# Optimization experiments

Measured on AMD Instinct MI355X. Metric: run time of the kernel, lower is better.

The kernel has to match this reference:

```python
import jax, jax.numpy as jnp
import numpy as np

N, E, D = 50000, 500000, 128


def layer_norm(x, w, b, eps=1e-5):
    mu = jnp.mean(x, axis=-1, keepdims=True)
    var = jnp.var(x, axis=-1, keepdims=True)
    return (x - mu) * jax.lax.rsqrt(var + eps) * w + b


def setup_inputs() -> dict:
    key = jax.random.key(0)
    ks = jax.random.split(key, 8)
    z = jax.random.normal(ks[0], (N, D), dtype=jnp.float32)
    pot_arcs = jax.random.randint(ks[1], (E, 2), 0, N, dtype=jnp.int64)
    s = 1.0 / np.sqrt(D)
    lin1_w = jax.random.uniform(ks[2], (D, D), jnp.float32, -s, s)
    lin1_b = jax.random.uniform(ks[3], (D,), jnp.float32, -s, s)
    lin2_w = jax.random.uniform(ks[4], (D, D), jnp.float32, -s, s)
    lin2_b = jax.random.uniform(ks[5], (D,), jnp.float32, -s, s)
    bil_w = jax.random.uniform(ks[6], (1, D, D), jnp.float32, -s, s)
    bil_b = jax.random.uniform(ks[7], (1,), jnp.float32, -s, s)
    norm_w = jnp.ones((D,), jnp.float32)
    norm_b = jnp.zeros((D,), jnp.float32)
    return {"z": z, "pot_arcs": pot_arcs, "lin1_w": lin1_w, "lin1_b": lin1_b,
            "lin2_w": lin2_w, "lin2_b": lin2_b, "bil_w": bil_w, "bil_b": bil_b,
            "norm_w": norm_w, "norm_b": norm_b}


def reference(z, pot_arcs, lin1_w, lin1_b, lin2_w, lin2_b, bil_w, bil_b, norm_w, norm_b):
    # shared LayerNorm on all nodes
    zn = layer_norm(z, norm_w, norm_b)                     # [N, D]
    x1 = zn[pot_arcs[:, 0]]                                # [E, D] gather heads
    x2 = zn[pot_arcs[:, 1]]                                # [E, D] gather tails
    # lin -> relu -> layernorm (dropout = identity at eval)
    h1 = layer_norm(jax.nn.relu(x1 @ lin1_w.T + lin1_b), norm_w, norm_b)
    h2 = layer_norm(jax.nn.relu(x2 @ lin2_w.T + lin2_b), norm_w, norm_b)
    # bilinear score: out_e = h1_e^T W h2_e + b, W = bil_w[0]
    score = jnp.einsum('ed,df,ef->e', h1, bil_w[0], h2) + bil_b[0]
    return score                                           # [E]
```

## Files before the change

### kernel.cpp

```cpp
#include <hip/hip_runtime.h>

#define D 128
#define TM 64

typedef __attribute__((ext_vector_type(8))) short short8v;
typedef __attribute__((ext_vector_type(4))) float float4v;

__device__ __forceinline__ unsigned short f2bf(float f) {
    unsigned int u = __float_as_uint(f);
    u += 0x7FFFu + ((u >> 16) & 1u);
    return (unsigned short)(u >> 16);
}
__device__ __forceinline__ float bflo(int u) {
    return __uint_as_float(((unsigned int)u) << 16);
}
__device__ __forceinline__ float bfhi(int u) {
    return __uint_as_float(((unsigned int)u) & 0xFFFF0000u);
}

__global__ __launch_bounds__(256) void wconv(
    const float* __restrict__ w1, const float* __restrict__ w2,
    const float* __restrict__ wb, unsigned short* __restrict__ dst)
{
    int tid = blockIdx.x * 256 + threadIdx.x;
    int w = tid >> 11;
    int r = tid & 2047;
    int l = r & 63;
    int tk = r >> 6;
    int t = tk >> 2, ks = tk & 3;
    int n = t * 16 + (l & 15);
    int k = ks * 32 + (l >> 4) * 8;
    const float* src = (w == 0) ? w1 : (w == 1) ? w2 : wb;
    const float* p = src + n * D + k;
    float4 a = *(const float4*)p;
    float4 b = *(const float4*)(p + 4);
    union { int4 i4; unsigned short u[8]; } pk;
    pk.u[0] = f2bf(a.x); pk.u[1] = f2bf(a.y); pk.u[2] = f2bf(a.z); pk.u[3] = f2bf(a.w);
    pk.u[4] = f2bf(b.x); pk.u[5] = f2bf(b.y); pk.u[6] = f2bf(b.z); pk.u[7] = f2bf(b.w);
    *(int4*)(dst + (size_t)tid * 8) = pk.i4;
}

__global__ __launch_bounds__(256) void node_kernel(
    const float* __restrict__ z,
    const unsigned short* __restrict__ wfrag,
    const float* __restrict__ lin1_b, const float* __restrict__ lin2_b,
    const float* __restrict__ norm_w, const float* __restrict__ norm_b,
    unsigned short* __restrict__ T1, unsigned short* __restrict__ T2,
    int N)
{
    __shared__ unsigned short sa[TM][136];
    __shared__ unsigned short sh[TM][136];

    const int tid   = threadIdx.x;
    const int lane  = tid & 63;
    const int wave  = tid >> 6;
    const int n0    = blockIdx.x * TM;
    const int cg    = lane & 15;
    const int q     = lane >> 4;
    const int rbase = wave * 16;

    {
        const int c = cg * 8;
        float4 nw0 = *(const float4*)(norm_w + c);
        float4 nw1 = *(const float4*)(norm_w + c + 4);
        float4 nb0 = *(const float4*)(norm_b + c);
        float4 nb1 = *(const float4*)(norm_b + c + 4);
        #pragma unroll
        for (int it = 0; it < 4; ++it) {
            int rr = rbase + it * 4 + q;
            int n  = n0 + rr;
            int nc = (n < N) ? n : (N - 1);
            const float* zp = z + (size_t)nc * D + c;
            float4 v0 = *(const float4*)zp;
            float4 v1 = *(const float4*)(zp + 4);
            float s  = v0.x + v0.y + v0.z + v0.w + v1.x + v1.y + v1.z + v1.w;
            float qq = v0.x*v0.x + v0.y*v0.y + v0.z*v0.z + v0.w*v0.w
                     + v1.x*v1.x + v1.y*v1.y + v1.z*v1.z + v1.w*v1.w;
            #pragma unroll
            for (int m = 1; m <= 8; m <<= 1) {
                s  += __shfl_xor(s, m, 64);
                qq += __shfl_xor(qq, m, 64);
            }
            float mu  = s * (1.0f / D);
            float var = qq * (1.0f / D) - mu * mu;
            float rs  = rsqrtf(var + 1e-5f);
            union { int4 i4; unsigned short u[8]; } pk;
            pk.u[0] = f2bf((v0.x - mu) * rs * nw0.x + nb0.x);
            pk.u[1] = f2bf((v0.y - mu) * rs * nw0.y + nb0.y);
            pk.u[2] = f2bf((v0.z - mu) * rs * nw0.z + nb0.z);
            pk.u[3] = f2bf((v0.w - mu) * rs * nw0.w + nb0.w);
            pk.u[4] = f2bf((v1.x - mu) * rs * nw1.x + nb1.x);
            pk.u[5] = f2bf((v1.y - mu) * rs * nw1.y + nb1.y);
            pk.u[6] = f2bf((v1.z - mu) * rs * nw1.z + nb1.z);
            pk.u[7] = f2bf((v1.w - mu) * rs * nw1.w + nb1.w);
            *(int4*)&sa[rr][c] = pk.i4;
        }
    }

    float4v acc1[8], acc2[8];
    #pragma unroll
    for (int t = 0; t < 8; ++t) { acc1[t] = (float4v)(0.0f); acc2[t] = (float4v)(0.0f); }
    #pragma unroll
    for (int ks = 0; ks < 4; ++ks) {
        short8v a = *(const short8v*)&sa[rbase + cg][ks * 32 + q * 8];
        const short8v* wp = (const short8v*)wfrag + ks * 64 + lane;
        #pragma unroll
        for (int t = 0; t < 8; ++t) {
            acc1[t] = __builtin_amdgcn_mfma_f32_16x16x32_bf16(a, wp[t * 256],        acc1[t], 0, 0, 0);
            acc2[t] = __builtin_amdgcn_mfma_f32_16x16x32_bf16(a, wp[t * 256 + 2048], acc2[t], 0, 0, 0);
        }
    }

    auto epilogue = [&](float4v* acc, const float* lb, unsigned short (*dst)[136]) {
        float s[4] = {0, 0, 0, 0}, qs[4] = {0, 0, 0, 0};
        #pragma unroll
        for (int t = 0; t < 8; ++t) {
            float b = lb[t * 16 + cg];
            #pragma unroll
            for (int i = 0; i < 4; ++i) {
                float v = fmaxf(acc[t][i] + b, 0.0f);
                acc[t][i] = v;
                s[i] += v; qs[i] += v * v;
            }
        }
        #pragma unroll
        for (int i = 0; i < 4; ++i) {
            #pragma unroll
            for (int m = 1; m <= 8; m <<= 1) {
                s[i]  += __shfl_xor(s[i], m, 64);
                qs[i] += __shfl_xor(qs[i], m, 64);
            }
            float mu  = s[i] * (1.0f / D);
            float var = qs[i] * (1.0f / D) - mu * mu;
            s[i] = mu; qs[i] = rsqrtf(var + 1e-5f);
        }
        #pragma unroll
        for (int t = 0; t < 8; ++t) {
            int col = t * 16 + cg;
            float nw = norm_w[col], nb = norm_b[col];
            #pragma unroll
            for (int i = 0; i < 4; ++i)
                dst[rbase + q * 4 + i][col] = f2bf((acc[t][i] - s[i]) * qs[i] * nw + nb);
        }
    };

    auto copyout = [&](const unsigned short (*S)[136], unsigned short* dst) {
        int r = tid >> 2;
        int n = n0 + r;
        if (n < N) {
            #pragma unroll
            for (int j = 0; j < 4; ++j) {
                int c = (tid & 3) * 8 + j * 32;
                *(int4*)(dst + (size_t)n * D + c) = *(const int4*)&S[r][c];
            }
        }
    };

    epilogue(acc1, lin1_b, sh);
    copyout(sh, T1);
    epilogue(acc2, lin2_b, sa);

    #pragma unroll
    for (int t = 0; t < 8; ++t) acc1[t] = (float4v)(0.0f);
    #pragma unroll
    for (int ks = 0; ks < 4; ++ks) {
        short8v a = *(const short8v*)&sa[rbase + cg][ks * 32 + q * 8];
        const short8v* wp = (const short8v*)wfrag + 4096 + ks * 64 + lane;
        #pragma unroll
        for (int t = 0; t < 8; ++t)
            acc1[t] = __builtin_amdgcn_mfma_f32_16x16x32_bf16(a, wp[t * 256], acc1[t], 0, 0, 0);
    }
    #pragma unroll
    for (int t = 0; t < 8; ++t)
        #pragma unroll
        for (int i = 0; i < 4; ++i)
            sh[rbase + q * 4 + i][t * 16 + cg] = f2bf(acc1[t][i]);
    copyout(sh, T2);
}

__global__ __launch_bounds__(256) void arc_kernel(
    const int* __restrict__ arcs,
    const unsigned short* __restrict__ T1,
    const unsigned short* __restrict__ T2,
    const float* __restrict__ bil_b,
    float* __restrict__ out, int E)
{
    const int tid  = threadIdx.x;
    const int lane = tid & 63;
    long long gw = ((long long)blockIdx.x * 256 + tid) >> 6;
    long long e0 = gw * 32;
    int aidx = lane >> 2;
    int s    = lane & 3;

    long long ii = e0 * 2 + lane;
    long long iimax = (long long)E * 2 - 1;
    int iv = arcs[ii <= iimax ? ii : iimax];
    int a0A = __shfl(iv, aidx * 2, 64);
    int a1A = __shfl(iv, aidx * 2 + 1, 64);
    int a0B = __shfl(iv, 32 + aidx * 2, 64);
    int a1B = __shfl(iv, 32 + aidx * 2 + 1, 64);
    long long eA = e0 + aidx;
    long long eB = e0 + 16 + aidx;

    const int4* PA = (const int4*)(T1 + (size_t)a0A * D);
    const int4* QA = (const int4*)(T2 + (size_t)a1A * D);
    const int4* PB = (const int4*)(T1 + (size_t)a0B * D);
    const int4* QB = (const int4*)(T2 + (size_t)a1B * D);
    int4 xa0 = PA[s], xa1 = PA[s + 4], xa2 = PA[s + 8], xa3 = PA[s + 12];
    int4 ya0 = QA[s], ya1 = QA[s + 4], ya2 = QA[s + 8], ya3 = QA[s + 12];
    int4 xb0 = PB[s], xb1 = PB[s + 4], xb2 = PB[s + 8], xb3 = PB[s + 12];
    int4 yb0 = QB[s], yb1 = QB[s + 4], yb2 = QB[s + 8], yb3 = QB[s + 12];

    #define DOT4(a, b) (bflo(a.x)*bflo(b.x) + bfhi(a.x)*bfhi(b.x) + \
                        bflo(a.y)*bflo(b.y) + bfhi(a.y)*bfhi(b.y) + \
                        bflo(a.z)*bflo(b.z) + bfhi(a.z)*bfhi(b.z) + \
                        bflo(a.w)*bflo(b.w) + bfhi(a.w)*bfhi(b.w))

    float accA = 0.0f, accB = 0.0f;
    accA += DOT4(xa0, ya0); accA += DOT4(xa1, ya1);
    accA += DOT4(xa2, ya2); accA += DOT4(xa3, ya3);
    accB += DOT4(xb0, yb0); accB += DOT4(xb1, yb1);
    accB += DOT4(xb2, yb2); accB += DOT4(xb3, yb3);
    #undef DOT4

    accA += __shfl_xor(accA, 1, 64);
    accA += __shfl_xor(accA, 2, 64);
    accB += __shfl_xor(accB, 1, 64);
    accB += __shfl_xor(accB, 2, 64);

    if (s == 0) {
        float bb = bil_b[0];
        if (eA < E) out[eA] = accA + bb;
        if (eB < E) out[eB] = accB + bb;
    }
}

extern "C" void kernel_launch(void* const* d_in, const int* in_sizes, int n_in,
                              void* d_out, int out_size, void* d_ws, size_t ws_size,
                              hipStream_t stream) {
    const float* z      = (const float*)d_in[0];
    const int*   arcs   = (const int*)d_in[1];
    const float* lin1_w = (const float*)d_in[2];
    const float* lin1_b = (const float*)d_in[3];
    const float* lin2_w = (const float*)d_in[4];
    const float* lin2_b = (const float*)d_in[5];
    const float* bil_w  = (const float*)d_in[6];
    const float* bil_b  = (const float*)d_in[7];
    const float* norm_w = (const float*)d_in[8];
    const float* norm_b = (const float*)d_in[9];
    float* out = (float*)d_out;

    const int N = in_sizes[0] / D;
    const int E = in_sizes[1] / 2;

    unsigned short* wfrag = (unsigned short*)d_ws;
    unsigned short* T1 = wfrag + 3 * 16384;
    unsigned short* T2 = T1 + (size_t)N * D;

    wconv<<<24, 256, 0, stream>>>(lin1_w, lin2_w, bil_w, wfrag);

    node_kernel<<<(N + TM - 1) / TM, 256, 0, stream>>>(
        z, wfrag, lin1_b, lin2_b, norm_w, norm_b, T1, T2, N);

    long long waves = ((long long)E + 31) / 32;
    int blocks = (int)((waves + 3) / 4);
    arc_kernel<<<blocks, 256, 0, stream>>>(arcs, T1, T2, bil_b, out, E);
}
```

Baseline: 143.8 us.

## Double node-kernel row tile so each wave reuses weight fragments across two row tiles

Raises the node kernel's row tile from 64 to 128, so each wave computes two 16-row MFMA tiles. Each weight fragment loaded from global is then reused for both tiles, roughly halving weight traffic per node. The separate shared staging buffer is removed and the single buffer is reused for the epilogue and copy-out, which keeps LDS use flat. The costs are doubled accumulator register pressure and half as many blocks, which may leave the GPU less occupied for N=50000.

```diff
diff --git a/kernel.cpp b/kernel.cpp
--- a/kernel.cpp
+++ b/kernel.cpp
@@ -1,7 +1,7 @@
 #include <hip/hip_runtime.h>
 
 #define D 128
-#define TM 64
+#define TM 128
 
 typedef __attribute__((ext_vector_type(8))) short short8v;
 typedef __attribute__((ext_vector_type(4))) float float4v;
@@ -49,7 +49,6 @@
     int N)
 {
     __shared__ unsigned short sa[TM][136];
-    __shared__ unsigned short sh[TM][136];
 
     const int tid   = threadIdx.x;
     const int lane  = tid & 63;
@@ -57,7 +56,7 @@
     const int n0    = blockIdx.x * TM;
     const int cg    = lane & 15;
     const int q     = lane >> 4;
-    const int rbase = wave * 16;
+    const int rbase = wave * 32;
 
     {
         const int c = cg * 8;
@@ -66,7 +65,7 @@
         float4 nb0 = *(const float4*)(norm_b + c);
         float4 nb1 = *(const float4*)(norm_b + c + 4);
         #pragma unroll
-        for (int it = 0; it < 4; ++it) {
+        for (int it = 0; it < 8; ++it) {
             int rr = rbase + it * 4 + q;
             int n  = n0 + rr;
             int nc = (n < N) ? n : (N - 1);
@@ -97,29 +96,36 @@
         }
     }
 
-    float4v acc1[8], acc2[8];
-    #pragma unroll
-    for (int t = 0; t < 8; ++t) { acc1[t] = (float4v)(0.0f); acc2[t] = (float4v)(0.0f); }
+    float4v acc1[2][8], acc2[2][8];
+    #pragma unroll
+    for (int rt = 0; rt < 2; ++rt)
+        #pragma unroll
+        for (int t = 0; t < 8; ++t) { acc1[rt][t] = (float4v)(0.0f); acc2[rt][t] = (float4v)(0.0f); }
     #pragma unroll
     for (int ks = 0; ks < 4; ++ks) {
-        short8v a = *(const short8v*)&sa[rbase + cg][ks * 32 + q * 8];
+        short8v a0 = *(const short8v*)&sa[rbase + cg][ks * 32 + q * 8];
+        short8v a1 = *(const short8v*)&sa[rbase + 16 + cg][ks * 32 + q * 8];
         const short8v* wp = (const short8v*)wfrag + ks * 64 + lane;
         #pragma unroll
         for (int t = 0; t < 8; ++t) {
-            acc1[t] = __builtin_amdgcn_mfma_f32_16x16x32_bf16(a, wp[t * 256],        acc1[t], 0, 0, 0);
-            acc2[t] = __builtin_amdgcn_mfma_f32_16x16x32_bf16(a, wp[t * 256 + 2048], acc2[t], 0, 0, 0);
-        }
-    }
-
-    auto epilogue = [&](float4v* acc, const float* lb, unsigned short (*dst)[136]) {
+            short8v b1 = wp[t * 256];
+            acc1[0][t] = __builtin_amdgcn_mfma_f32_16x16x32_bf16(a0, b1, acc1[0][t], 0, 0, 0);
+            acc1[1][t] = __builtin_amdgcn_mfma_f32_16x16x32_bf16(a1, b1, acc1[1][t], 0, 0, 0);
+            short8v b2 = wp[t * 256 + 2048];
+            acc2[0][t] = __builtin_amdgcn_mfma_f32_16x16x32_bf16(a0, b2, acc2[0][t], 0, 0, 0);
+            acc2[1][t] = __builtin_amdgcn_mfma_f32_16x16x32_bf16(a1, b2, acc2[1][t], 0, 0, 0);
+        }
+    }
+
+    auto epilogue = [&](float4v (*acc)[8], int rt, const float* lb) {
         float s[4] = {0, 0, 0, 0}, qs[4] = {0, 0, 0, 0};
         #pragma unroll
         for (int t = 0; t < 8; ++t) {
             float b = lb[t * 16 + cg];
             #pragma unroll
             for (int i = 0; i < 4; ++i) {
-                float v = fmaxf(acc[t][i] + b, 0.0f);
-                acc[t][i] = v;
+                float v = fmaxf(acc[rt][t][i] + b, 0.0f);
+                acc[rt][t][i] = v;
                 s[i] += v; qs[i] += v * v;
             }
         }
@@ -140,42 +146,53 @@
             float nw = norm_w[col], nb = norm_b[col];
             #pragma unroll
             for (int i = 0; i < 4; ++i)
-                dst[rbase + q * 4 + i][col] = f2bf((acc[t][i] - s[i]) * qs[i] * nw + nb);
+                sa[rbase + rt * 16 + q * 4 + i][col] =
+                    f2bf((acc[rt][t][i] - s[i]) * qs[i] * nw + nb);
         }
     };
 
-    auto copyout = [&](const unsigned short (*S)[136], unsigned short* dst) {
-        int r = tid >> 2;
+    auto copyout = [&](unsigned short* dst) {
+        int r = tid >> 1;
         int n = n0 + r;
         if (n < N) {
             #pragma unroll
-            for (int j = 0; j < 4; ++j) {
-                int c = (tid & 3) * 8 + j * 32;
-                *(int4*)(dst + (size_t)n * D + c) = *(const int4*)&S[r][c];
+            for (int j = 0; j < 8; ++j) {
+                int c = (tid & 1) * 8 + j * 16;
+                *(int4*)(dst + (size_t)n * D + c) = *(const int4*)&sa[r][c];
             }
         }
     };
 
-    epilogue(acc1, lin1_b, sh);
-    copyout(sh, T1);
-    epilogue(acc2, lin2_b, sa);
-
-    #pragma unroll
-    for (int t = 0; t < 8; ++t) acc1[t] = (float4v)(0.0f);
+    epilogue(acc1, 0, lin1_b);
+    epilogue(acc1, 1, lin1_b);
+    copyout(T1);
+    epilogue(acc2, 0, lin2_b);
+    epilogue(acc2, 1, lin2_b);
+
+    #pragma unroll
+    for (int rt = 0; rt < 2; ++rt)
+        #pragma unroll
+        for (int t = 0; t < 8; ++t) acc1[rt][t] = (float4v)(0.0f);
     #pragma unroll
     for (int ks = 0; ks < 4; ++ks) {
-        short8v a = *(const short8v*)&sa[rbase + cg][ks * 32 + q * 8];
+        short8v a0 = *(const short8v*)&sa[rbase + cg][ks * 32 + q * 8];
+        short8v a1 = *(const short8v*)&sa[rbase + 16 + cg][ks * 32 + q * 8];
         const short8v* wp = (const short8v*)wfrag + 4096 + ks * 64 + lane;
         #pragma unroll
+        for (int t = 0; t < 8; ++t) {
+            short8v b = wp[t * 256];
+            acc1[0][t] = __builtin_amdgcn_mfma_f32_16x16x32_bf16(a0, b, acc1[0][t], 0, 0, 0);
+            acc1[1][t] = __builtin_amdgcn_mfma_f32_16x16x32_bf16(a1, b, acc1[1][t], 0, 0, 0);
+        }
+    }
+    #pragma unroll
+    for (int rt = 0; rt < 2; ++rt)
+        #pragma unroll
         for (int t = 0; t < 8; ++t)
-            acc1[t] = __builtin_amdgcn_mfma_f32_16x16x32_bf16(a, wp[t * 256], acc1[t], 0, 0, 0);
-    }
-    #pragma unroll
-    for (int t = 0; t < 8; ++t)
-        #pragma unroll
-        for (int i = 0; i < 4; ++i)
-            sh[rbase + q * 4 + i][t * 16 + cg] = f2bf(acc1[t][i]);
-    copyout(sh, T2);
+            #pragma unroll
+            for (int i = 0; i < 4; ++i)
+                sa[rbase + rt * 16 + q * 4 + i][t * 16 + cg] = f2bf(acc1[rt][t][i]);
+    copyout(T2);
 }
 
 __global__ __launch_bounds__(256) void arc_kernel(
```

Result: slower. 156.4 us (+8.7%).
